# Kernel optimization log

Hardware: AMD Instinct MI355X
Metric: run time of the kernel (lower is better)

The kernel has to match this reference:

```python
import jax, jax.numpy as jnp
import numpy as np

B, N, D, H = 2, 2048, 1024, 16
DH = D // H


def setup_inputs() -> dict:
    key = jax.random.key(0)
    ks = jax.random.split(key, 5)
    s = 0.02
    return {
        "x": jax.random.normal(ks[0], (B, N, D), dtype=jnp.float32),
        "Wq": jax.random.normal(ks[1], (D, D), dtype=jnp.float32) * s,
        "Wk": jax.random.normal(ks[2], (D, D), dtype=jnp.float32) * s,
        "Wv": jax.random.normal(ks[3], (D, D), dtype=jnp.float32) * s,
        "Wo": jax.random.normal(ks[4], (D, D), dtype=jnp.float32) * s,
        "bo": jnp.zeros((D,), dtype=jnp.float32),
    }


def reference(x, Wq, Wk, Wv, Wo, bo):
    b, n, d = x.shape
    # linear projections (torch Linear: y = x @ W.T), split into heads -> [b,h,n,dh]
    def proj(W):
        return jnp.einsum('bnd,ed->bne', x, W).reshape(b, n, H, DH).transpose(0, 2, 1, 3)
    q, k, v = proj(Wq), proj(Wk), proj(Wv)
    scores = jnp.einsum('bhqd,bhkd->bhqk', q, k)  # [b,h,n,n]
    causal = jnp.triu(jnp.ones((n, n), dtype=bool), k=1)
    scores = jnp.where(causal, -jnp.inf, scores)
    # NOTE: module scales by 1/sqrt(num_key_tokens), not 1/sqrt(d_head)
    w = jax.nn.softmax(scores / jnp.sqrt(jnp.float32(n)), axis=-1)
    ctx = jnp.einsum('bhqk,bhkd->bhqd', w, v)
    ctx = ctx.transpose(0, 2, 1, 3).reshape(b, n, d)
    return jnp.einsum('bnd,ed->bne', ctx, Wo) + bo
```

## Files before the change

### kernel.cpp

```cpp
#include <hip/hip_runtime.h>
#include <hip/hip_bf16.h>

typedef __attribute__((ext_vector_type(8))) short bf16x8;
typedef __attribute__((ext_vector_type(4))) float f32x4;
typedef unsigned short u16;

__device__ __forceinline__ u16 f2bf(float f) {
  union { float f; unsigned int u; } v; v.f = f;
  return (u16)((v.u + 0x7fffu + ((v.u >> 16) & 1u)) >> 16);
}
__device__ __forceinline__ unsigned int pack_bf2(float f0, float f1) {
  union { float f; unsigned int u; } a, b; a.f = f0; b.f = f1;
  return __builtin_amdgcn_perm(b.u + 0x8000u, a.u + 0x8000u, 0x07060302u);
}

#define GLOAD_LDS16(g, l) __builtin_amdgcn_global_load_lds( \
    (const __attribute__((address_space(1))) void*)(g),     \
    (__attribute__((address_space(3))) void*)(l), 16, 0, 0)

__global__ __launch_bounds__(256) void conv_all(const float* __restrict__ x,
                                                const float* __restrict__ wq, const float* __restrict__ wk,
                                                const float* __restrict__ wv, const float* __restrict__ wo,
                                                u16* __restrict__ xb, u16* __restrict__ qo, u16* __restrict__ ko,
                                                u16* __restrict__ vo, u16* __restrict__ oo) {
  int y = blockIdx.y;
  const float* src; u16* dst;
  if (y < 4) { src = x + (size_t)y * 1048576; dst = xb + (size_t)y * 1048576; }
  else if (y == 4) { src = wq; dst = qo; }
  else if (y == 5) { src = wk; dst = ko; }
  else if (y == 6) { src = wv; dst = vo; }
  else { src = wo; dst = oo; }
  int i = (blockIdx.x * 256 + threadIdx.x) * 4;
  float4 v = *(const float4*)(src + i);
  ushort4 o;
  o.x = f2bf(v.x); o.y = f2bf(v.y); o.z = f2bf(v.z); o.w = f2bf(v.w);
  *(ushort4*)(dst + i) = o;
}

template <bool SW>
__device__ __forceinline__ void gemm_main(const u16* __restrict__ A, const u16* __restrict__ W,
                                          u16* As, u16* Bs, int m0, int n0, int K,
                                          f32x4 acc[4][4]) {
  int tid = threadIdx.x, wave = tid >> 6, lane = tid & 63;
  int lane15 = lane & 15, quad = lane >> 4;
  int wm = (wave >> 1) * 64, wn = (wave & 1) * 64;
  for (int k0 = 0; k0 < K; k0 += 64) {
    __syncthreads();
#pragma unroll
    for (int i = 0; i < 4; i++) {
      int rbase = wave * 32 + i * 8;
      int rloc = rbase + (lane >> 3);
      int ca = ((lane & 7) ^ (rloc & 7)) * 8;
      GLOAD_LDS16(A + (size_t)(m0 + rloc) * K + k0 + ca, As + rbase * 64);
      GLOAD_LDS16(W + (size_t)(n0 + rloc) * K + k0 + ca, Bs + rbase * 64);
    }
    __syncthreads();
#pragma unroll
    for (int kc = 0; kc < 2; kc++) {
      bf16x8 a[4], b[4];
#pragma unroll
      for (int mi = 0; mi < 4; mi++) {
        int m = wm + mi * 16 + lane15;
        a[mi] = *(const bf16x8*)(As + m * 64 + (((kc * 4 + quad) ^ (m & 7)) * 8));
      }
#pragma unroll
      for (int ni = 0; ni < 4; ni++) {
        int n = wn + ni * 16 + lane15;
        b[ni] = *(const bf16x8*)(Bs + n * 64 + (((kc * 4 + quad) ^ (n & 7)) * 8));
      }
#pragma unroll
      for (int mi = 0; mi < 4; mi++)
#pragma unroll
        for (int ni = 0; ni < 4; ni++)
          acc[mi][ni] = SW ? __builtin_amdgcn_mfma_f32_16x16x32_bf16(b[ni], a[mi], acc[mi][ni], 0, 0, 0)
                           : __builtin_amdgcn_mfma_f32_16x16x32_bf16(a[mi], b[ni], acc[mi][ni], 0, 0, 0);
    }
  }
}

__global__ __launch_bounds__(256, 3) void gemm_qkv(const u16* __restrict__ xb,
                                                   const u16* __restrict__ wq, const u16* __restrict__ wk,
                                                   const u16* __restrict__ wv,
                                                   u16* __restrict__ Qb, u16* __restrict__ Kb,
                                                   u16* __restrict__ Vtg) {
  __shared__ __align__(16) u16 As[128 * 64];
  __shared__ __align__(16) u16 Bs[128 * 64];
  const int K = 1024;
  int z = blockIdx.z;
  const u16* W = (z == 0) ? wq : (z == 1) ? wk : wv;
  int m0 = blockIdx.x * 128, n0 = blockIdx.y * 128;
  f32x4 acc[4][4];
#pragma unroll
  for (int i = 0; i < 4; i++)
#pragma unroll
    for (int j = 0; j < 4; j++) acc[i][j] = (f32x4){0.f, 0.f, 0.f, 0.f};

  int tid = threadIdx.x, wave = tid >> 6, lane = tid & 63;
  int lane15 = lane & 15, quad = lane >> 4;
  int wm = (wave >> 1) * 64, wn = (wave & 1) * 64;
  const float kQs = 0.022097086912079608f * 1.4426950408889634f;

  if (z < 2) {
    gemm_main<true>(xb, W, As, Bs, m0, n0, K, acc);
    u16* Out = z ? Kb : Qb;
    float sc = z ? 1.0f : kQs;
#pragma unroll
    for (int mi = 0; mi < 4; mi++)
#pragma unroll
      for (int ni = 0; ni < 4; ni++) {
        int token = m0 + wm + mi * 16 + lane15;
        int fb = n0 + wn + ni * 16 + quad * 4;
        ushort4 o;
        o.x = f2bf(acc[mi][ni][0] * sc); o.y = f2bf(acc[mi][ni][1] * sc);
        o.z = f2bf(acc[mi][ni][2] * sc); o.w = f2bf(acc[mi][ni][3] * sc);
        *(ushort4*)&Out[(size_t)token * 1024 + fb] = o;
      }
  } else {
    gemm_main<false>(xb, W, As, Bs, m0, n0, K, acc);
#pragma unroll
    for (int mi = 0; mi < 4; mi++)
#pragma unroll
      for (int ni = 0; ni < 4; ni++) {
        int row = m0 + wm + mi * 16 + quad * 4;
        int col = n0 + wn + ni * 16 + lane15;
        int bb = row >> 11, nn = row & 2047;
        ushort4 o;
        o.x = f2bf(acc[mi][ni][0]); o.y = f2bf(acc[mi][ni][1]);
        o.z = f2bf(acc[mi][ni][2]); o.w = f2bf(acc[mi][ni][3]);
        *(ushort4*)&Vtg[(size_t)(bb * 1024 + col) * 2048 + nn] = o;
      }
  }
}

__global__ __launch_bounds__(256, 2) void gemm_out(const u16* __restrict__ A, const u16* __restrict__ W,
                                                   float* __restrict__ Of, const float* __restrict__ bias) {
  __shared__ __align__(16) u16 As[128 * 64];
  __shared__ __align__(16) u16 Bs[64 * 64];
  const int K = 1024;
  int m0 = blockIdx.x * 128, n0 = blockIdx.y * 64;
  int tid = threadIdx.x, wave = tid >> 6, lane = tid & 63;
  int lane15 = lane & 15, quad = lane >> 4;
  int wm = (wave >> 1) * 64, wn = (wave & 1) * 32;
  f32x4 acc[4][2];
#pragma unroll
  for (int i = 0; i < 4; i++)
#pragma unroll
    for (int j = 0; j < 2; j++) acc[i][j] = (f32x4){0.f, 0.f, 0.f, 0.f};
  for (int k0 = 0; k0 < K; k0 += 64) {
    __syncthreads();
#pragma unroll
    for (int i = 0; i < 4; i++) {
      int rbase = wave * 32 + i * 8;
      int rloc = rbase + (lane >> 3);
      int ca = ((lane & 7) ^ (rloc & 7)) * 8;
      GLOAD_LDS16(A + (size_t)(m0 + rloc) * K + k0 + ca, As + rbase * 64);
    }
#pragma unroll
    for (int i = 0; i < 2; i++) {
      int rbase = wave * 16 + i * 8;
      int rloc = rbase + (lane >> 3);
      int ca = ((lane & 7) ^ (rloc & 7)) * 8;
      GLOAD_LDS16(W + (size_t)(n0 + rloc) * K + k0 + ca, Bs + rbase * 64);
    }
    __syncthreads();
#pragma unroll
    for (int kc = 0; kc < 2; kc++) {
      bf16x8 a[4], b[2];
#pragma unroll
      for (int mi = 0; mi < 4; mi++) {
        int m = wm + mi * 16 + lane15;
        a[mi] = *(const bf16x8*)(As + m * 64 + (((kc * 4 + quad) ^ (m & 7)) * 8));
      }
#pragma unroll
      for (int ni = 0; ni < 2; ni++) {
        int n = wn + ni * 16 + lane15;
        b[ni] = *(const bf16x8*)(Bs + n * 64 + (((kc * 4 + quad) ^ (n & 7)) * 8));
      }
#pragma unroll
      for (int mi = 0; mi < 4; mi++)
#pragma unroll
        for (int ni = 0; ni < 2; ni++)
          acc[mi][ni] = __builtin_amdgcn_mfma_f32_16x16x32_bf16(b[ni], a[mi], acc[mi][ni], 0, 0, 0);
    }
  }
#pragma unroll
  for (int mi = 0; mi < 4; mi++)
#pragma unroll
    for (int ni = 0; ni < 2; ni++) {
      int token = m0 + wm + mi * 16 + lane15;
      int fb = n0 + wn + ni * 16 + quad * 4;
      float4 bb = *(const float4*)&bias[fb];
      float4 o;
      o.x = acc[mi][ni][0] + bb.x; o.y = acc[mi][ni][1] + bb.y;
      o.z = acc[mi][ni][2] + bb.z; o.w = acc[mi][ni][3] + bb.w;
      *(float4*)&Of[(size_t)token * 1024 + fb] = o;
    }
}

__global__ __launch_bounds__(256, 4) void attn5(const u16* __restrict__ Q, const u16* __restrict__ Kg,
                                                const u16* __restrict__ Vtg, u16* __restrict__ ctx) {
  __shared__ __align__(16) u16 Ks[2][64 * 64];
  __shared__ __align__(16) u16 Vts[2][64 * 64];
  __shared__ __align__(16) u16 Ps[64 * 64];
  int tid = threadIdx.x, wave = tid >> 6, lane = tid & 63;
  int lane15 = lane & 15, quad = lane >> 4;

  int sidx = 31 - blockIdx.x;
  int bh = blockIdx.y;
  int b = bh >> 4, h = bh & 15;
  int qbase = sidx * 64;

  bf16x8 qb[2];
#pragma unroll
  for (int kc = 0; kc < 2; kc++)
    qb[kc] = *(const bf16x8*)&Q[(size_t)(b * 2048 + qbase + wave * 16 + lane15) * 1024 +
                                h * 64 + kc * 32 + quad * 8];

  f32x4 oacc[4];
#pragma unroll
  for (int c4 = 0; c4 < 4; c4++) oacc[c4] = (f32x4){0.f, 0.f, 0.f, 0.f};
  float lsum = 0.f;

  auto stage = [&](int t, int d) {
    int tb = t * 64;
#pragma unroll
    for (int i = 0; i < 2; i++) {
      int rbase = wave * 16 + i * 8;
      int rk = rbase + (lane >> 3);
      int ca = ((lane & 7) ^ (rk & 7)) * 8;
      GLOAD_LDS16(&Kg[(size_t)(b * 2048 + tb + rk) * 1024 + h * 64 + ca], &Ks[d][rbase * 64]);
      GLOAD_LDS16(&Vtg[(size_t)(b * 1024 + h * 64 + rk) * 2048 + tb + ca], &Vts[d][rbase * 64]);
    }
  };

  int sw = (lane15 & 7) << 1;
  int prow = wave * 16 + lane15;

  stage(0, 0);
  for (int t = 0; t <= sidx; ++t) {
    __syncthreads();
    if (t < sidx) stage(t + 1, (t + 1) & 1);
    int d = t & 1;

    f32x4 s4[4];
#pragma unroll
    for (int ct = 0; ct < 4; ct++) {
      int kr = ct * 16 + lane15;
      const u16* kp = &Ks[d][kr * 64];
      bf16x8 ka0 = *(const bf16x8*)(kp + ((quad ^ (kr & 7)) * 8));
      bf16x8 ka1 = *(const bf16x8*)(kp + (((4 + quad) ^ (kr & 7)) * 8));
      f32x4 z = (f32x4){0.f, 0.f, 0.f, 0.f};
      z = __builtin_amdgcn_mfma_f32_16x16x32_bf16(ka0, qb[0], z, 0, 0, 0);
      z = __builtin_amdgcn_mfma_f32_16x16x32_bf16(ka1, qb[1], z, 0, 0, 0);
      s4[ct] = z;
    }
    if (t == sidx) {
      int ql = wave * 16 + lane15;
#pragma unroll
      for (int ct = 0; ct < 4; ct++)
#pragma unroll
        for (int r = 0; r < 4; r++)
          if (ct * 16 + quad * 4 + r > ql) s4[ct][r] = -10000.0f;
    }
#pragma unroll
    for (int ct = 0; ct < 4; ct++)
#pragma unroll
      for (int r = 0; r < 4; r++) {
        float p = __builtin_amdgcn_exp2f(s4[ct][r]);
        s4[ct][r] = p; lsum += p;
      }
#pragma unroll
    for (int ct = 0; ct < 4; ct++) {
      unsigned int lo = pack_bf2(s4[ct][0], s4[ct][1]);
      unsigned int hi = pack_bf2(s4[ct][2], s4[ct][3]);
      int u = (ct * 4 + quad) ^ sw;
      *(uint2*)&Ps[prow * 64 + u * 4] = (uint2){lo, hi};
    }
#pragma unroll
    for (int kc = 0; kc < 2; kc++) {
      int up = (kc * 8 + quad * 2) ^ sw;
      bf16x8 pb = *(const bf16x8*)&Ps[prow * 64 + up * 4];
#pragma unroll
      for (int c4 = 0; c4 < 4; c4++) {
        int dh = c4 * 16 + lane15;
        bf16x8 va = *(const bf16x8*)&Vts[d][dh * 64 + (((kc * 4 + quad) ^ (dh & 7)) * 8)];
        oacc[c4] = __builtin_amdgcn_mfma_f32_16x16x32_bf16(va, pb, oacc[c4], 0, 0, 0);
      }
    }
  }

  lsum += __shfl_xor(lsum, 16);
  lsum += __shfl_xor(lsum, 32);
  float inv = 1.0f / lsum;

  size_t off = (size_t)(b * 2048 + qbase + wave * 16 + lane15) * 1024 + h * 64;
#pragma unroll
  for (int c4 = 0; c4 < 4; c4++) {
    ushort4 o;
    o.x = f2bf(oacc[c4][0] * inv); o.y = f2bf(oacc[c4][1] * inv);
    o.z = f2bf(oacc[c4][2] * inv); o.w = f2bf(oacc[c4][3] * inv);
    *(ushort4*)&ctx[off + c4 * 16 + quad * 4] = o;
  }
}

extern "C" void kernel_launch(void* const* d_in, const int* in_sizes, int n_in,
                              void* d_out, int out_size, void* d_ws, size_t ws_size,
                              hipStream_t stream) {
  const float* x  = (const float*)d_in[0];
  const float* Wq = (const float*)d_in[1];
  const float* Wk = (const float*)d_in[2];
  const float* Wv = (const float*)d_in[3];
  const float* Wo = (const float*)d_in[4];
  const float* bo = (const float*)d_in[5];
  float* out = (float*)d_out;
  char* ws = (char*)d_ws;
  const size_t MB = 1024 * 1024;
  u16* xb   = (u16*)(ws);
  u16* wqb  = (u16*)(ws +  8 * MB);
  u16* wkb  = (u16*)(ws + 10 * MB);
  u16* wvb  = (u16*)(ws + 12 * MB);
  u16* wob  = (u16*)(ws + 14 * MB);
  u16* Qb   = (u16*)(ws + 16 * MB);
  u16* Kb   = (u16*)(ws + 24 * MB);
  u16* Vtg  = (u16*)(ws + 32 * MB);
  u16* ctxb = (u16*)(ws + 40 * MB);

  conv_all<<<dim3(1024, 8), 256, 0, stream>>>(x, Wq, Wk, Wv, Wo, xb, wqb, wkb, wvb, wob);
  gemm_qkv<<<dim3(32, 8, 3), 256, 0, stream>>>(xb, wqb, wkb, wvb, Qb, Kb, Vtg);
  attn5<<<dim3(32, 32), 256, 0, stream>>>(Qb, Kb, Vtg, ctxb);
  gemm_out<<<dim3(32, 16), 256, 0, stream>>>(ctxb, wob, out, bo);
}
```

Measured before the change: 184.7 us.

## Pair causal query tiles per block and split KV across waves with 32x32 MFMA

```diff
diff --git a/kernel.cpp b/kernel.cpp
--- a/kernel.cpp
+++ b/kernel.cpp
@@ -3,6 +3,7 @@
 
 typedef __attribute__((ext_vector_type(8))) short bf16x8;
 typedef __attribute__((ext_vector_type(4))) float f32x4;
+typedef __attribute__((ext_vector_type(16))) float f32x16;
 typedef unsigned short u16;
 
 __device__ __forceinline__ u16 f2bf(float f) {
@@ -197,109 +198,161 @@
     }
 }
 
-__global__ __launch_bounds__(256, 4) void attn5(const u16* __restrict__ Q, const u16* __restrict__ Kg,
+__global__ __launch_bounds__(256, 2) void attn6(const u16* __restrict__ Q, const u16* __restrict__ Kg,
                                                 const u16* __restrict__ Vtg, u16* __restrict__ ctx) {
-  __shared__ __align__(16) u16 Ks[2][64 * 64];
-  __shared__ __align__(16) u16 Vts[2][64 * 64];
-  __shared__ __align__(16) u16 Ps[64 * 64];
+  __shared__ __align__(16) u16 SH[24576];
   int tid = threadIdx.x, wave = tid >> 6, lane = tid & 63;
-  int lane15 = lane & 15, quad = lane >> 4;
-
-  int sidx = 31 - blockIdx.x;
-  int bh = blockIdx.y;
+  int l31 = lane & 31, hf = lane >> 5;
+  int qt = wave & 1, kvh = wave >> 1;
+
+  int g = blockIdx.x, bh = blockIdx.y;
   int b = bh >> 4, h = bh & 15;
-  int qbase = sidx * 64;
-
-  bf16x8 qb[2];
-#pragma unroll
-  for (int kc = 0; kc < 2; kc++)
-    qb[kc] = *(const bf16x8*)&Q[(size_t)(b * 2048 + qbase + wave * 16 + lane15) * 1024 +
-                                h * 64 + kc * 32 + quad * 8];
-
-  f32x4 oacc[4];
-#pragma unroll
-  for (int c4 = 0; c4 < 4; c4++) oacc[c4] = (f32x4){0.f, 0.f, 0.f, 0.f};
-  float lsum = 0.f;
+  int tA = g, tB = 31 - g;
+  int qbase[2] = {g * 64, (31 - g) * 64};
+
+  bf16x8 qb[2][4];
+#pragma unroll
+  for (int st = 0; st < 2; st++)
+#pragma unroll
+    for (int s = 0; s < 4; s++)
+      qb[st][s] = *(const bf16x8*)&Q[(size_t)(b * 2048 + qbase[st] + qt * 32 + l31) * 1024 +
+                                     h * 64 + s * 16 + hf * 8];
+
+  f32x16 oacc[2][2];
+#pragma unroll
+  for (int st = 0; st < 2; st++)
+#pragma unroll
+    for (int dt = 0; dt < 2; dt++)
+#pragma unroll
+      for (int r = 0; r < 16; r++) oacc[st][dt][r] = 0.f;
+  float lsum[2] = {0.f, 0.f};
 
   auto stage = [&](int t, int d) {
     int tb = t * 64;
+    u16* Kd = SH + d * 4096;
+    u16* Vd = SH + 8192 + d * 4096;
 #pragma unroll
     for (int i = 0; i < 2; i++) {
       int rbase = wave * 16 + i * 8;
       int rk = rbase + (lane >> 3);
       int ca = ((lane & 7) ^ (rk & 7)) * 8;
-      GLOAD_LDS16(&Kg[(size_t)(b * 2048 + tb + rk) * 1024 + h * 64 + ca], &Ks[d][rbase * 64]);
-      GLOAD_LDS16(&Vtg[(size_t)(b * 1024 + h * 64 + rk) * 2048 + tb + ca], &Vts[d][rbase * 64]);
+      GLOAD_LDS16(&Kg[(size_t)(b * 2048 + tb + rk) * 1024 + h * 64 + ca], Kd + rbase * 64);
+      GLOAD_LDS16(&Vtg[(size_t)(b * 1024 + h * 64 + rk) * 2048 + tb + ca], Vd + rbase * 64);
     }
   };
 
-  int sw = (lane15 & 7) << 1;
-  int prow = wave * 16 + lane15;
+  u16* Ps = SH + 16384;
+  int psw = (l31 & 3) << 1;
 
   stage(0, 0);
-  for (int t = 0; t <= sidx; ++t) {
-    __syncthreads();
-    if (t < sidx) stage(t + 1, (t + 1) & 1);
+  for (int t = 0; t <= tB; ++t) {
+    __syncthreads();
+    if (t < tB) stage(t + 1, (t + 1) & 1);
     int d = t & 1;
-
-    f32x4 s4[4];
-#pragma unroll
-    for (int ct = 0; ct < 4; ct++) {
-      int kr = ct * 16 + lane15;
-      const u16* kp = &Ks[d][kr * 64];
-      bf16x8 ka0 = *(const bf16x8*)(kp + ((quad ^ (kr & 7)) * 8));
-      bf16x8 ka1 = *(const bf16x8*)(kp + (((4 + quad) ^ (kr & 7)) * 8));
-      f32x4 z = (f32x4){0.f, 0.f, 0.f, 0.f};
-      z = __builtin_amdgcn_mfma_f32_16x16x32_bf16(ka0, qb[0], z, 0, 0, 0);
-      z = __builtin_amdgcn_mfma_f32_16x16x32_bf16(ka1, qb[1], z, 0, 0, 0);
-      s4[ct] = z;
-    }
-    if (t == sidx) {
-      int ql = wave * 16 + lane15;
-#pragma unroll
-      for (int ct = 0; ct < 4; ct++)
-#pragma unroll
-        for (int r = 0; r < 4; r++)
-          if (ct * 16 + quad * 4 + r > ql) s4[ct][r] = -10000.0f;
-    }
-#pragma unroll
-    for (int ct = 0; ct < 4; ct++)
-#pragma unroll
-      for (int r = 0; r < 4; r++) {
-        float p = __builtin_amdgcn_exp2f(s4[ct][r]);
-        s4[ct][r] = p; lsum += p;
-      }
-#pragma unroll
-    for (int ct = 0; ct < 4; ct++) {
-      unsigned int lo = pack_bf2(s4[ct][0], s4[ct][1]);
-      unsigned int hi = pack_bf2(s4[ct][2], s4[ct][3]);
-      int u = (ct * 4 + quad) ^ sw;
-      *(uint2*)&Ps[prow * 64 + u * 4] = (uint2){lo, hi};
-    }
-#pragma unroll
-    for (int kc = 0; kc < 2; kc++) {
-      int up = (kc * 8 + quad * 2) ^ sw;
-      bf16x8 pb = *(const bf16x8*)&Ps[prow * 64 + up * 4];
-#pragma unroll
-      for (int c4 = 0; c4 < 4; c4++) {
-        int dh = c4 * 16 + lane15;
-        bf16x8 va = *(const bf16x8*)&Vts[d][dh * 64 + (((kc * 4 + quad) ^ (dh & 7)) * 8)];
-        oacc[c4] = __builtin_amdgcn_mfma_f32_16x16x32_bf16(va, pb, oacc[c4], 0, 0, 0);
-      }
-    }
-  }
-
-  lsum += __shfl_xor(lsum, 16);
-  lsum += __shfl_xor(lsum, 32);
-  float inv = 1.0f / lsum;
-
-  size_t off = (size_t)(b * 2048 + qbase + wave * 16 + lane15) * 1024 + h * 64;
-#pragma unroll
-  for (int c4 = 0; c4 < 4; c4++) {
-    ushort4 o;
-    o.x = f2bf(oacc[c4][0] * inv); o.y = f2bf(oacc[c4][1] * inv);
-    o.z = f2bf(oacc[c4][2] * inv); o.w = f2bf(oacc[c4][3] * inv);
-    *(ushort4*)&ctx[off + c4 * 16 + quad * 4] = o;
+    const u16* Kd = SH + d * 4096;
+    const u16* Vd = SH + 8192 + d * 4096;
+
+    int krow = kvh * 32 + l31;
+    const u16* kp = Kd + krow * 64;
+    bf16x8 kf[4];
+#pragma unroll
+    for (int s = 0; s < 4; s++)
+      kf[s] = *(const bf16x8*)(kp + (((2 * s + hf) ^ (krow & 7)) * 8));
+    bf16x8 vf[2][2];
+#pragma unroll
+    for (int dt = 0; dt < 2; dt++) {
+      int vrow = dt * 32 + l31;
+#pragma unroll
+      for (int c = 0; c < 2; c++)
+        vf[dt][c] = *(const bf16x8*)(Vd + vrow * 64 + (((4 * kvh + 2 * c + hf) ^ (vrow & 7)) * 8));
+    }
+
+#pragma unroll
+    for (int st = 0; st < 2; st++) {
+      bool active = st ? true : (t <= tA);
+      bool diag = st ? (t == tB) : (t == tA);
+      if (!active) continue;
+      if (diag && kvh > qt) continue;
+
+      f32x16 sv;
+#pragma unroll
+      for (int r = 0; r < 16; r++) sv[r] = 0.f;
+#pragma unroll
+      for (int s = 0; s < 4; s++)
+        sv = __builtin_amdgcn_mfma_f32_32x32x16_bf16(kf[s], qb[st][s], sv, 0, 0, 0);
+
+      if (diag && kvh == qt) {
+#pragma unroll
+        for (int r = 0; r < 16; r++) {
+          int kvloc = (r & 3) + 8 * (r >> 2) + 4 * hf;
+          if (kvloc > l31) sv[r] = -10000.0f;
+        }
+      }
+#pragma unroll
+      for (int r = 0; r < 16; r++) {
+        float p = __builtin_amdgcn_exp2f(sv[r]);
+        sv[r] = p; lsum[st] += p;
+      }
+      u16* pr = Ps + (wave * 2 + st) * 1024 + l31 * 32;
+#pragma unroll
+      for (int gr = 0; gr < 4; gr++) {
+        unsigned int lo = pack_bf2(sv[4 * gr + 0], sv[4 * gr + 1]);
+        unsigned int hi = pack_bf2(sv[4 * gr + 2], sv[4 * gr + 3]);
+        int u = (2 * gr + hf) ^ psw;
+        *(uint2*)(pr + u * 4) = (uint2){lo, hi};
+      }
+#pragma unroll
+      for (int c = 0; c < 2; c++) {
+        int u0 = (4 * c + 2 * hf) ^ psw;
+        bf16x8 pf = *(const bf16x8*)(pr + u0 * 4);
+#pragma unroll
+        for (int dt = 0; dt < 2; dt++)
+          oacc[st][dt] = __builtin_amdgcn_mfma_f32_32x32x16_bf16(vf[dt][c], pf, oacc[st][dt], 0, 0, 0);
+      }
+    }
+  }
+
+  lsum[0] += __shfl_xor(lsum[0], 32);
+  lsum[1] += __shfl_xor(lsum[1], 32);
+  float* MG = (float*)SH;
+  float* LS = (float*)(SH + 16384);
+  __syncthreads();
+  if (kvh == 1) {
+#pragma unroll
+    for (int st = 0; st < 2; st++) {
+#pragma unroll
+      for (int dt = 0; dt < 2; dt++) {
+        float* p = MG + (((qt * 2 + st) * 2 + dt) * 64 + lane) * 16;
+#pragma unroll
+        for (int q4 = 0; q4 < 4; q4++)
+          *(f32x4*)(p + q4 * 4) = (f32x4){oacc[st][dt][4 * q4], oacc[st][dt][4 * q4 + 1],
+                                          oacc[st][dt][4 * q4 + 2], oacc[st][dt][4 * q4 + 3]};
+      }
+      LS[(qt * 2 + st) * 32 + l31] = lsum[st];
+    }
+  }
+  __syncthreads();
+  if (kvh == 0) {
+#pragma unroll
+    for (int st = 0; st < 2; st++) {
+      float inv = 1.0f / (lsum[st] + LS[(qt * 2 + st) * 32 + l31]);
+      int token = qbase[st] + qt * 32 + l31;
+      size_t off = (size_t)(b * 2048 + token) * 1024 + h * 64;
+#pragma unroll
+      for (int dt = 0; dt < 2; dt++) {
+        const float* p = MG + (((qt * 2 + st) * 2 + dt) * 64 + lane) * 16;
+#pragma unroll
+        for (int gr = 0; gr < 4; gr++) {
+          f32x4 m = *(const f32x4*)(p + gr * 4);
+          ushort4 o;
+          o.x = f2bf((oacc[st][dt][4 * gr + 0] + m[0]) * inv);
+          o.y = f2bf((oacc[st][dt][4 * gr + 1] + m[1]) * inv);
+          o.z = f2bf((oacc[st][dt][4 * gr + 2] + m[2]) * inv);
+          o.w = f2bf((oacc[st][dt][4 * gr + 3] + m[3]) * inv);
+          *(ushort4*)&ctx[off + dt * 32 + 8 * gr + 4 * hf] = o;
+        }
+      }
+    }
   }
 }
 
@@ -327,6 +380,6 @@
 
   conv_all<<<dim3(1024, 8), 256, 0, stream>>>(x, Wq, Wk, Wv, Wo, xb, wqb, wkb, wvb, wob);
   gemm_qkv<<<dim3(32, 8, 3), 256, 0, stream>>>(xb, wqb, wkb, wvb, Qb, Kb, Vtg);
-  attn5<<<dim3(32, 32), 256, 0, stream>>>(Qb, Kb, Vtg, ctxb);
+  attn6<<<dim3(16, 32), 256, 0, stream>>>(Qb, Kb, Vtg, ctxb);
   gemm_out<<<dim3(32, 16), 256, 0, stream>>>(ctxb, wob, out, bo);
 }
```

After: 173.2 us. 6.2% less time.
